# Kernel optimization log

Measured on AMD Instinct MI355X. Metric: run time of the kernel, lower is better.

Reference implementation:

```python
import jax, jax.numpy as jnp
import numpy as np

B, S, H, NH = 4, 2048, 1024, 16
D = H // NH  # head_dim = 64


def setup_inputs() -> dict:
    key = jax.random.key(0)
    ks = jax.random.split(key, 8)
    hidden_states = jax.random.normal(ks[0], (B, S, H), dtype=jnp.float32)
    attention_mask = jnp.zeros((B, 1, 1, S), dtype=jnp.float32)  # additive, bidirectional
    # RoPE tables (cos/sin per position, full head_dim)
    inv_freq = 1.0 / (10000.0 ** (jnp.arange(0, D, 2, dtype=jnp.float32) / D))
    t = jnp.arange(S, dtype=jnp.float32)
    freqs = jnp.outer(t, inv_freq)              # [S, D/2]
    emb = jnp.concatenate([freqs, freqs], -1)   # [S, D]
    cos, sin = jnp.cos(emb), jnp.sin(emb)
    scale = 1.0 / np.sqrt(H)
    Wq = jax.random.normal(ks[1], (H, H), dtype=jnp.float32) * scale
    Wk = jax.random.normal(ks[2], (H, H), dtype=jnp.float32) * scale
    Wv = jax.random.normal(ks[3], (H, H), dtype=jnp.float32) * scale
    Wo = jax.random.normal(ks[4], (H, H), dtype=jnp.float32) * scale
    return {"hidden_states": hidden_states, "attention_mask": attention_mask,
            "cos": cos, "sin": sin, "Wq": Wq, "Wk": Wk, "Wv": Wv, "Wo": Wo}


def _rotate_half(x):
    x1, x2 = jnp.split(x, 2, axis=-1)
    return jnp.concatenate([-x2, x1], axis=-1)


def _rope(x, cos, sin):
    # x: [B, NH, S, D]; cos/sin: [S, D]
    c = cos[None, None, :, :]
    s = sin[None, None, :, :]
    return x * c + _rotate_half(x) * s


def reference(hidden_states, attention_mask, cos, sin, Wq, Wk, Wv, Wo):
    b, s, h = hidden_states.shape
    # QKV projections (torch Linear: x @ W^T)
    def proj(W):
        y = jnp.einsum('bsh,oh->bso', hidden_states, W)
        return y.reshape(b, s, NH, D).transpose(0, 2, 1, 3)  # [B, NH, S, D]
    q, k, v = proj(Wq), proj(Wk), proj(Wv)
    q = _rope(q, cos, sin)
    k = _rope(k, cos, sin)
    scale = D ** -0.5
    scores = jnp.einsum('bhqd,bhkd->bhqk', q, k) * scale + attention_mask
    attn = jax.nn.softmax(scores, axis=-1)
    out = jnp.einsum('bhqk,bhkd->bhqd', attn, v)            # [B, NH, S, D]
    out = out.transpose(0, 2, 1, 3).reshape(b, s, h)        # [B, S, H]
    return jnp.einsum('bsh,oh->bso', out, Wo)
```

## Files before the change

### kernel.cpp

```cpp
#include <hip/hip_runtime.h>


typedef __bf16 bf16x8 __attribute__((ext_vector_type(8)));
typedef float f32x4 __attribute__((ext_vector_type(4)));
typedef float f32x16 __attribute__((ext_vector_type(16)));
typedef unsigned short u16x8 __attribute__((ext_vector_type(8)));
typedef unsigned short u16x4 __attribute__((ext_vector_type(4)));
typedef const __attribute__((address_space(1))) void* gptr_t;
typedef __attribute__((address_space(3))) void* lptr_t;

template <int N> struct ic { static constexpr int v = N; };

__device__ __forceinline__ unsigned short f2bf(float f) {
  union { float f; unsigned u; } v; v.f = f;
  unsigned r = (v.u + 0x7fffu + ((v.u >> 16) & 1u)) >> 16;
  return (unsigned short)r;
}

__device__ __forceinline__ unsigned short f2bfn(float f) {
  union { __bf16 h; unsigned short u; } v;
  v.h = (__bf16)f;
  return v.u;
}

__device__ __forceinline__ unsigned cvtpk(float lo, float hi_) {
  unsigned r;
  asm("v_cvt_pk_bf16_f32 %0, %1, %2" : "=v"(r) : "v"(lo), "v"(hi_));
  return r;
}

__device__ __forceinline__ void gld16(const void* g, void* l) {
  __builtin_amdgcn_global_load_lds((gptr_t)g, (lptr_t)l, 16, 0, 0);
}

__global__ __launch_bounds__(256) void cvt_all(
    const float* __restrict__ hidden, const float* __restrict__ Wq,
    const float* __restrict__ Wk, const float* __restrict__ Wv,
    const float* __restrict__ Wo, unsigned short* __restrict__ Xb,
    unsigned short* __restrict__ Wb) {
  size_t i8 = ((size_t)blockIdx.x * 256 + threadIdx.x) * 8;
  const float* src;
  unsigned short* dst;
  if (i8 < 8388608) {
    src = hidden + i8;
    dst = Xb + i8;
  } else {
    size_t r = i8 - 8388608;
    int wsel = (int)(r >> 20);
    size_t off = r & 1048575;
    const float* wsrc = (wsel == 0) ? Wq : (wsel == 1) ? Wk : (wsel == 2) ? Wv : Wo;
    src = wsrc + off;
    dst = Wb + r;
  }
  f32x4 a = *(const f32x4*)(src);
  f32x4 b = *(const f32x4*)(src + 4);
  u16x8 o;
  o[0] = f2bf(a[0]); o[1] = f2bf(a[1]); o[2] = f2bf(a[2]); o[3] = f2bf(a[3]);
  o[4] = f2bf(b[0]); o[5] = f2bf(b[1]); o[6] = f2bf(b[2]); o[7] = f2bf(b[3]);
  *(u16x8*)dst = o;
}

__global__ __launch_bounds__(256, 3) void gemm_k(
    const unsigned short* __restrict__ A,
    const unsigned short* __restrict__ W0, const unsigned short* __restrict__ W1,
    const unsigned short* __restrict__ W2,
    const float* __restrict__ cosT, const float* __restrict__ sinT,
    unsigned short* __restrict__ Qh, unsigned short* __restrict__ Kh,
    unsigned short* __restrict__ Vh, float* __restrict__ Cout, int mode) {
  __shared__ char sm[32768];
  char* As = sm;
  char* Bs = sm + 16384;
  const int tid = threadIdx.x, lane = tid & 63, w = tid >> 6;
  const int wm = w >> 1, wn = w & 1;
  const int brow = blockIdx.y * 128;
  const int bcol = blockIdx.x * 128;
  const unsigned short* Wsel =
      (mode == 0) ? W0 : (blockIdx.z == 0 ? W0 : (blockIdx.z == 1 ? W1 : W2));

  f32x4 acc[4][4];
#pragma unroll
  for (int m = 0; m < 4; ++m)
#pragma unroll
    for (int n = 0; n < 4; ++n) acc[m][n] = (f32x4){0.f, 0.f, 0.f, 0.f};

  const char* Abase = (const char*)A + (size_t)brow * 2048;
  const char* Bbase = (const char*)Wsel + (size_t)bcol * 2048;

  for (int kt = 0; kt < 1024; kt += 64) {
#pragma unroll
    for (int c = 0; c < 4; ++c) {
      int Lb = w * 4096 + c * 1024;
      int L = Lb + lane * 16;
      int r = L >> 7, kb = L & 127;
      int sw = kb ^ ((r & 7) << 4);
      gld16(Abase + (size_t)r * 2048 + kt * 2 + sw, As + Lb);
      gld16(Bbase + (size_t)r * 2048 + kt * 2 + sw, Bs + Lb);
    }
    __syncthreads();
#pragma unroll
    for (int kk = 0; kk < 2; ++kk) {
      int kb = kk * 64 + (lane >> 4) * 16;
      bf16x8 af[4], bfr[4];
#pragma unroll
      for (int m = 0; m < 4; ++m) {
        int r = wm * 64 + m * 16 + (lane & 15);
        af[m] = *(const bf16x8*)(As + r * 128 + (kb ^ ((r & 7) << 4)));
      }
#pragma unroll
      for (int n = 0; n < 4; ++n) {
        int r = wn * 64 + n * 16 + (lane & 15);
        bfr[n] = *(const bf16x8*)(Bs + r * 128 + (kb ^ ((r & 7) << 4)));
      }
#pragma unroll
      for (int m = 0; m < 4; ++m)
#pragma unroll
        for (int n = 0; n < 4; ++n)
          acc[m][n] = __builtin_amdgcn_mfma_f32_16x16x32_bf16(af[m], bfr[n],
                                                              acc[m][n], 0, 0, 0);
    }
    __syncthreads();
  }

  if (mode == 0) {
#pragma unroll
    for (int m = 0; m < 4; ++m)
#pragma unroll
      for (int n = 0; n < 4; ++n)
#pragma unroll
        for (int i = 0; i < 4; ++i) {
          int row = brow + wm * 64 + m * 16 + (lane >> 4) * 4 + i;
          int col = bcol + wn * 64 + n * 16 + (lane & 15);
          Cout[(size_t)row * 1024 + col] = acc[m][n][i];
        }
  } else {
    const int z = blockIdx.z;
    const int h = (bcol + wn * 64) >> 6;
    if (z == 2) {
#pragma unroll
      for (int m = 0; m < 4; ++m) {
        int row0 = brow + wm * 64 + m * 16 + (lane >> 4) * 4;
        int b = row0 >> 11, s0 = row0 & 2047;
        size_t base = (size_t)(b * 16 + h) * 64 * 2048 + s0;
#pragma unroll
        for (int n = 0; n < 4; ++n) {
          int dl = n * 16 + (lane & 15);
          u16x4 pw;
#pragma unroll
          for (int i = 0; i < 4; ++i) pw[i] = f2bf(acc[m][n][i]);
          *(u16x4*)(Vh + base + (size_t)dl * 2048) = pw;
        }
      }
    } else {
      unsigned short* dst = (z == 0) ? Qh : Kh;
      const float qs = (z == 0) ? 0.18033688f : 1.0f;
#pragma unroll
      for (int m = 0; m < 4; ++m)
#pragma unroll
        for (int i = 0; i < 4; ++i) {
          int row = brow + wm * 64 + m * 16 + (lane >> 4) * 4 + i;
          int b = row >> 11, s = row & 2047;
          size_t hb2 = ((size_t)(b * 16 + h) * 2048 + s) * 64;
#pragma unroll
          for (int n = 0; n < 2; ++n) {
            int dl = n * 16 + (lane & 15);
            float c = cosT[s * 64 + dl], sn = sinT[s * 64 + dl];
            float lo = acc[m][n][i], hi = acc[m][n + 2][i];
            dst[hb2 + dl] = f2bf((lo * c - hi * sn) * qs);
            dst[hb2 + dl + 32] = f2bf((hi * c + lo * sn) * qs);
          }
        }
    }
  }
}

__global__ __launch_bounds__(256, 4) void attn_k(
    const unsigned short* __restrict__ Q, const unsigned short* __restrict__ K,
    const unsigned short* __restrict__ Vt, const float* __restrict__ mask,
    unsigned short* __restrict__ O) {
  __shared__ char Ks[2][8192];
  __shared__ char Vs[2][8192];
  __shared__ float l_arr[4][32];
  const int tid = threadIdx.x, lane = tid & 63, w = tid >> 6;
  const int q31 = lane & 31, hi = lane >> 5;
  const int wg = blockIdx.x;
  const int work = (wg & 7) * 128 + (wg >> 3);
  const int qt = work & 15, hl = work >> 4;
  const int h = hl & 15, b = hl >> 4;
  const size_t hb = (size_t)(b * 16 + h) * (2048 * 64);
  const int q0 = qt * 128 + w * 32;
  const float L2E = 1.44269504f;
  const float MREF = 12.0f;
  const int rdo = q31 * 32 + hi * 16;

  bf16x8 qb[4];
  {
    const char* qrow = (const char*)(Q + hb + (size_t)(q0 + q31) * 64);
#pragma unroll
    for (int ks = 0; ks < 4; ++ks)
      qb[ks] = *(const bf16x8*)(qrow + ks * 32 + hi * 16);
  }

  float l_part = 0.f;
  f32x16 oacc[2];
#pragma unroll
  for (int e = 0; e < 16; ++e) { oacc[0][e] = 0.f; oacc[1][e] = 0.f; }

  int koff0, koff1, vof0, vof1;
  {
    int L0 = w * 2048 + lane * 16;
    int c0 = L0 >> 12, ks0 = (L0 >> 10) & 3, q0l = (L0 >> 5) & 31,
        hi0 = (L0 >> 4) & 1;
    int row0 = c0 * 32 + q0l, kb0 = ks0 * 32 + hi0 * 16;
    koff0 = row0 * 128 + kb0;
    vof0 = row0 * 4096 + kb0;
    int L1 = L0 + 1024;
    int c1 = L1 >> 12, ks1 = (L1 >> 10) & 3, q1l = (L1 >> 5) & 31,
        hi1 = (L1 >> 4) & 1;
    int row1 = c1 * 32 + q1l, kb1 = ks1 * 32 + hi1 * 16;
    koff1 = row1 * 128 + kb1;
    vof1 = row1 * 4096 + kb1;
  }
  const char* Kg = (const char*)(K + hb);
  const char* Vg = (const char*)(Vt + hb);
  const float* mp = mask + (size_t)b * 2048;

  gld16(Kg + koff0, Ks[0] + w * 2048);
  gld16(Kg + koff1, Ks[0] + w * 2048 + 1024);
  gld16(Vg + vof0, Vs[0] + w * 2048);
  gld16(Vg + vof1, Vs[0] + w * 2048 + 1024);
  __syncthreads();

  auto body = [&](auto curc, int t) {
    constexpr int cur = decltype(curc)::v;
    constexpr int nxt = 1 - cur;
    if (t < 31) {
      const char* kp = Kg + (size_t)(t + 1) * 8192;
      const char* vp = Vg + (size_t)(t + 1) * 128;
      gld16(kp + koff0, Ks[nxt] + w * 2048);
      gld16(kp + koff1, Ks[nxt] + w * 2048 + 1024);
      gld16(vp + vof0, Vs[nxt] + w * 2048);
      gld16(vp + vof1, Vs[nxt] + w * 2048 + 1024);
    }
    const float* mrow = mp + t * 64;

    f32x16 sacc[2];
#pragma unroll
    for (int c = 0; c < 2; ++c) {
#pragma unroll
      for (int g = 0; g < 4; ++g) {
        f32x4 mv = *(const f32x4*)(mrow + c * 32 + g * 8 + hi * 4);
#pragma unroll
        for (int i = 0; i < 4; ++i)
          sacc[c][g * 4 + i] = fmaf(mv[i], L2E, -MREF);
      }
      __builtin_amdgcn_s_setprio(1);
#pragma unroll
      for (int ks = 0; ks < 4; ++ks) {
        bf16x8 kf =
            *(const bf16x8*)(Ks[cur] + (c * 4 + ks) * 1024 + rdo);
        sacc[c] = __builtin_amdgcn_mfma_f32_32x32x16_bf16(kf, qb[ks], sacc[c],
                                                          0, 0, 0);
      }
      __builtin_amdgcn_s_setprio(0);
#pragma unroll
      for (int e = 0; e < 16; ++e)
        sacc[c][e] = __builtin_amdgcn_exp2f(sacc[c][e]);
      float s0 = (sacc[c][0] + sacc[c][1]) + (sacc[c][2] + sacc[c][3]);
      float s1 = (sacc[c][4] + sacc[c][5]) + (sacc[c][6] + sacc[c][7]);
      float s2 = (sacc[c][8] + sacc[c][9]) + (sacc[c][10] + sacc[c][11]);
      float s3 = (sacc[c][12] + sacc[c][13]) + (sacc[c][14] + sacc[c][15]);
      l_part += (s0 + s1) + (s2 + s3);
    }

    __builtin_amdgcn_s_setprio(1);
#pragma unroll
    for (int c = 0; c < 2; ++c) {
#pragma unroll
      for (int par = 0; par < 2; ++par) {
        const int t2 = c * 2 + par;
        unsigned a0 = cvtpk(sacc[c][par * 8 + 0], sacc[c][par * 8 + 1]);
        unsigned a1 = cvtpk(sacc[c][par * 8 + 2], sacc[c][par * 8 + 3]);
        unsigned b0 = cvtpk(sacc[c][par * 8 + 4], sacc[c][par * 8 + 5]);
        unsigned b1 = cvtpk(sacc[c][par * 8 + 6], sacc[c][par * 8 + 7]);
        asm("v_permlane32_swap_b32 %0, %1" : "+v"(a0), "+v"(b0));
        asm("v_permlane32_swap_b32 %0, %1" : "+v"(a1), "+v"(b1));
        union { unsigned u[4]; bf16x8 v; } pu;
        pu.u[0] = a0; pu.u[1] = a1; pu.u[2] = b0; pu.u[3] = b1;
        bf16x8 vf0 = *(const bf16x8*)(Vs[cur] + t2 * 1024 + rdo);
        bf16x8 vf1 = *(const bf16x8*)(Vs[cur] + 4096 + t2 * 1024 + rdo);
        oacc[0] = __builtin_amdgcn_mfma_f32_32x32x16_bf16(pu.v, vf0, oacc[0],
                                                          0, 0, 0);
        oacc[1] = __builtin_amdgcn_mfma_f32_32x32x16_bf16(pu.v, vf1, oacc[1],
                                                          0, 0, 0);
      }
    }
    __builtin_amdgcn_s_setprio(0);
    __syncthreads();
  };

  for (int t = 0; t < 32; t += 2) {
    body(ic<0>{}, t);
    body(ic<1>{}, t + 1);
  }

  float lr = l_part + __shfl_xor(l_part, 32, 64);
  l_arr[w][q31] = 1.0f / lr;

#pragma unroll
  for (int g = 0; g < 4; ++g) {
    f32x4 iv = *(const f32x4*)(&l_arr[w][g * 8 + hi * 4]);
    const int qrow = q0 + g * 8 + hi * 4;
#pragma unroll
    for (int i = 0; i < 4; ++i) {
      size_t rb = (size_t)(b * 2048 + qrow + i) * 1024 + h * 64;
      O[rb + q31] = f2bfn(oacc[0][g * 4 + i] * iv[i]);
      O[rb + 32 + q31] = f2bfn(oacc[1][g * 4 + i] * iv[i]);
    }
  }
}

extern "C" void kernel_launch(void* const* d_in, const int* in_sizes, int n_in,
                              void* d_out, int out_size, void* d_ws, size_t ws_size,
                              hipStream_t stream) {
  const float* hidden = (const float*)d_in[0];
  const float* amask = (const float*)d_in[1];
  const float* cosT = (const float*)d_in[2];
  const float* sinT = (const float*)d_in[3];
  const float* Wq = (const float*)d_in[4];
  const float* Wk = (const float*)d_in[5];
  const float* Wv = (const float*)d_in[6];
  const float* Wo = (const float*)d_in[7];
  float* out = (float*)d_out;

  if (ws_size < (size_t)92274688) return;
  unsigned short* Xb = (unsigned short*)d_ws;
  unsigned short* Wqb = Xb + (size_t)8192 * 1024;
  unsigned short* Wkb = Wqb + (size_t)1024 * 1024;
  unsigned short* Wvb = Wkb + (size_t)1024 * 1024;
  unsigned short* Wob = Wvb + (size_t)1024 * 1024;
  unsigned short* Qh = Wob + (size_t)1024 * 1024;
  unsigned short* Kh = Qh + (size_t)8388608;
  unsigned short* Vt = Kh + (size_t)8388608;
  unsigned short* Ob = Vt + (size_t)8388608;

  cvt_all<<<6144, 256, 0, stream>>>(hidden, Wq, Wk, Wv, Wo, Xb, Wqb);

  gemm_k<<<dim3(8, 64, 3), 256, 0, stream>>>(Xb, Wqb, Wkb, Wvb, cosT, sinT, Qh, Kh,
                                             Vt, nullptr, 1);
  attn_k<<<1024, 256, 0, stream>>>(Qh, Kh, Vt, amask, Ob);
  gemm_k<<<dim3(8, 64, 1), 256, 0, stream>>>(Ob, Wob, Wob, Wob, cosT, sinT, nullptr,
                                             nullptr, nullptr, out, 0);
}
```

Measured before the change: 212.4 us.

## Fuse Q/K/V projections into one 768-thread block sharing the A tile

Adds a dedicated QKV GEMM kernel in which each 768-thread block loads one 128x64 tile of the activation into LDS and three weight tiles, with four waves per projection. This removes the threefold re-read of the activation tile that happened when Q, K and V ran as separate grid-z blocks. The trade-off is 64KB of LDS and 768 threads per block, which limits occupancy, and the __launch_bounds__(768,3) request may constrain registers. The output projection kernel is simplified to remove the mode branch.

```diff
diff --git a/kernel.cpp b/kernel.cpp
--- a/kernel.cpp
+++ b/kernel.cpp
@@ -60,13 +60,124 @@
   *(u16x8*)dst = o;
 }
 
-__global__ __launch_bounds__(256, 3) void gemm_k(
+__global__ __launch_bounds__(768, 3) void gemm_qkv(
     const unsigned short* __restrict__ A,
     const unsigned short* __restrict__ W0, const unsigned short* __restrict__ W1,
     const unsigned short* __restrict__ W2,
     const float* __restrict__ cosT, const float* __restrict__ sinT,
     unsigned short* __restrict__ Qh, unsigned short* __restrict__ Kh,
-    unsigned short* __restrict__ Vh, float* __restrict__ Cout, int mode) {
+    unsigned short* __restrict__ Vh) {
+  __shared__ char sm[65536];
+  const int tid = threadIdx.x, lane = tid & 63, w = tid >> 6;
+  const int l15 = lane & 15, h2 = lane >> 4;
+  const int z = w >> 2, sub = w & 3;
+  const int wm = sub >> 1, wn = sub & 1;
+  const int brow = blockIdx.y * 128;
+  const int bcol = blockIdx.x * 128;
+
+  const char* Abase = (const char*)A + (size_t)brow * 2048;
+  const char* Wb0 = (const char*)W0 + (size_t)bcol * 2048;
+  const char* Wb1 = (const char*)W1 + (size_t)bcol * 2048;
+  const char* Wb2 = (const char*)W2 + (size_t)bcol * 2048;
+
+  const char* gsrc[6];
+  int gdst[6];
+#pragma unroll
+  for (int i = 0; i < 6; ++i) {
+    int g = tid + i * 768;
+    bool val = g < 4096;
+    int gg = val ? g : 0;
+    int r = (gg & 1023) >> 3;
+    int sw = ((gg & 7) * 16) ^ ((r & 7) << 4);
+    const char* base;
+    if (gg < 1024) base = Abase;
+    else {
+      int zz = (gg >> 10) - 1;
+      base = (zz == 0) ? Wb0 : (zz == 1 ? Wb1 : Wb2);
+    }
+    gsrc[i] = val ? (base + (size_t)r * 2048 + sw) : nullptr;
+    gdst[i] = gg * 16;
+  }
+
+  f32x4 acc[4][4];
+#pragma unroll
+  for (int m = 0; m < 4; ++m)
+#pragma unroll
+    for (int n = 0; n < 4; ++n) acc[m][n] = (f32x4){0.f, 0.f, 0.f, 0.f};
+
+  const char* Asw = sm;
+  const char* Bsw = sm + 16384 + z * 16384;
+
+  for (int kt = 0; kt < 16; ++kt) {
+#pragma unroll
+    for (int i = 0; i < 6; ++i)
+      if (gsrc[i]) gld16(gsrc[i] + kt * 128, sm + gdst[i]);
+    __syncthreads();
+#pragma unroll
+    for (int kk = 0; kk < 2; ++kk) {
+      int kb = kk * 64 + h2 * 16;
+      bf16x8 af[4], bfr[4];
+#pragma unroll
+      for (int m = 0; m < 4; ++m) {
+        int r = wm * 64 + m * 16 + l15;
+        af[m] = *(const bf16x8*)(Asw + r * 128 + (kb ^ ((r & 7) << 4)));
+      }
+#pragma unroll
+      for (int n = 0; n < 4; ++n) {
+        int r = wn * 64 + n * 16 + l15;
+        bfr[n] = *(const bf16x8*)(Bsw + r * 128 + (kb ^ ((r & 7) << 4)));
+      }
+#pragma unroll
+      for (int m = 0; m < 4; ++m)
+#pragma unroll
+        for (int n = 0; n < 4; ++n)
+          acc[m][n] = __builtin_amdgcn_mfma_f32_16x16x32_bf16(af[m], bfr[n],
+                                                              acc[m][n], 0, 0, 0);
+    }
+    __syncthreads();
+  }
+
+  const int h = blockIdx.x * 2 + wn;
+  if (z == 2) {
+#pragma unroll
+    for (int m = 0; m < 4; ++m) {
+      int row0 = brow + wm * 64 + m * 16 + h2 * 4;
+      int b = row0 >> 11, s0 = row0 & 2047;
+      size_t base = (size_t)(b * 16 + h) * 64 * 2048 + s0;
+#pragma unroll
+      for (int n = 0; n < 4; ++n) {
+        int dl = n * 16 + l15;
+        u16x4 pw;
+#pragma unroll
+        for (int i = 0; i < 4; ++i) pw[i] = f2bf(acc[m][n][i]);
+        *(u16x4*)(Vh + base + (size_t)dl * 2048) = pw;
+      }
+    }
+  } else {
+    unsigned short* dst = (z == 0) ? Qh : Kh;
+    const float qs = (z == 0) ? 0.18033688f : 1.0f;
+#pragma unroll
+    for (int m = 0; m < 4; ++m)
+#pragma unroll
+      for (int i = 0; i < 4; ++i) {
+        int row = brow + wm * 64 + m * 16 + h2 * 4 + i;
+        int b = row >> 11, s = row & 2047;
+        size_t hb2 = ((size_t)(b * 16 + h) * 2048 + s) * 64;
+#pragma unroll
+        for (int n = 0; n < 2; ++n) {
+          int dl = n * 16 + l15;
+          float c = cosT[s * 64 + dl], sn = sinT[s * 64 + dl];
+          float lo = acc[m][n][i], hi = acc[m][n + 2][i];
+          dst[hb2 + dl] = f2bf((lo * c - hi * sn) * qs);
+          dst[hb2 + dl + 32] = f2bf((hi * c + lo * sn) * qs);
+        }
+      }
+  }
+}
+
+__global__ __launch_bounds__(256, 3) void gemm_k(
+    const unsigned short* __restrict__ A, const unsigned short* __restrict__ W0,
+    float* __restrict__ Cout) {
   __shared__ char sm[32768];
   char* As = sm;
   char* Bs = sm + 16384;
@@ -74,8 +185,6 @@
   const int wm = w >> 1, wn = w & 1;
   const int brow = blockIdx.y * 128;
   const int bcol = blockIdx.x * 128;
-  const unsigned short* Wsel =
-      (mode == 0) ? W0 : (blockIdx.z == 0 ? W0 : (blockIdx.z == 1 ? W1 : W2));
 
   f32x4 acc[4][4];
 #pragma unroll
@@ -84,7 +193,7 @@
     for (int n = 0; n < 4; ++n) acc[m][n] = (f32x4){0.f, 0.f, 0.f, 0.f};
 
   const char* Abase = (const char*)A + (size_t)brow * 2048;
-  const char* Bbase = (const char*)Wsel + (size_t)bcol * 2048;
+  const char* Bbase = (const char*)W0 + (size_t)bcol * 2048;
 
   for (int kt = 0; kt < 1024; kt += 64) {
 #pragma unroll
@@ -121,56 +230,16 @@
     __syncthreads();
   }
 
-  if (mode == 0) {
-#pragma unroll
-    for (int m = 0; m < 4; ++m)
-#pragma unroll
-      for (int n = 0; n < 4; ++n)
-#pragma unroll
-        for (int i = 0; i < 4; ++i) {
-          int row = brow + wm * 64 + m * 16 + (lane >> 4) * 4 + i;
-          int col = bcol + wn * 64 + n * 16 + (lane & 15);
-          Cout[(size_t)row * 1024 + col] = acc[m][n][i];
-        }
-  } else {
-    const int z = blockIdx.z;
-    const int h = (bcol + wn * 64) >> 6;
-    if (z == 2) {
-#pragma unroll
-      for (int m = 0; m < 4; ++m) {
-        int row0 = brow + wm * 64 + m * 16 + (lane >> 4) * 4;
-        int b = row0 >> 11, s0 = row0 & 2047;
-        size_t base = (size_t)(b * 16 + h) * 64 * 2048 + s0;
-#pragma unroll
-        for (int n = 0; n < 4; ++n) {
-          int dl = n * 16 + (lane & 15);
-          u16x4 pw;
-#pragma unroll
-          for (int i = 0; i < 4; ++i) pw[i] = f2bf(acc[m][n][i]);
-          *(u16x4*)(Vh + base + (size_t)dl * 2048) = pw;
-        }
-      }
-    } else {
-      unsigned short* dst = (z == 0) ? Qh : Kh;
-      const float qs = (z == 0) ? 0.18033688f : 1.0f;
-#pragma unroll
-      for (int m = 0; m < 4; ++m)
-#pragma unroll
-        for (int i = 0; i < 4; ++i) {
-          int row = brow + wm * 64 + m * 16 + (lane >> 4) * 4 + i;
-          int b = row >> 11, s = row & 2047;
-          size_t hb2 = ((size_t)(b * 16 + h) * 2048 + s) * 64;
-#pragma unroll
-          for (int n = 0; n < 2; ++n) {
-            int dl = n * 16 + (lane & 15);
-            float c = cosT[s * 64 + dl], sn = sinT[s * 64 + dl];
-            float lo = acc[m][n][i], hi = acc[m][n + 2][i];
-            dst[hb2 + dl] = f2bf((lo * c - hi * sn) * qs);
-            dst[hb2 + dl + 32] = f2bf((hi * c + lo * sn) * qs);
-          }
-        }
-    }
-  }
+#pragma unroll
+  for (int m = 0; m < 4; ++m)
+#pragma unroll
+    for (int n = 0; n < 4; ++n)
+#pragma unroll
+      for (int i = 0; i < 4; ++i) {
+        int row = brow + wm * 64 + m * 16 + (lane >> 4) * 4 + i;
+        int col = bcol + wn * 64 + n * 16 + (lane & 15);
+        Cout[(size_t)row * 1024 + col] = acc[m][n][i];
+      }
 }
 
 __global__ __launch_bounds__(256, 4) void attn_k(
@@ -345,9 +414,8 @@
 
   cvt_all<<<6144, 256, 0, stream>>>(hidden, Wq, Wk, Wv, Wo, Xb, Wqb);
 
-  gemm_k<<<dim3(8, 64, 3), 256, 0, stream>>>(Xb, Wqb, Wkb, Wvb, cosT, sinT, Qh, Kh,
-                                             Vt, nullptr, 1);
+  gemm_qkv<<<dim3(8, 64), 768, 0, stream>>>(Xb, Wqb, Wkb, Wvb, cosT, sinT, Qh,
+                                            Kh, Vt);
   attn_k<<<1024, 256, 0, stream>>>(Qh, Kh, Vt, amask, Ob);
-  gemm_k<<<dim3(8, 64, 1), 256, 0, stream>>>(Ob, Wob, Wob, Wob, cosT, sinT, nullptr,
-                                             nullptr, nullptr, out, 0);
-}
+  gemm_k<<<dim3(8, 64), 256, 0, stream>>>(Ob, Wob, out);
+}
```

After: 201.2 us. 5.3% less time.
